# Kernel optimization log

Measured on AMD Instinct MI355X. Metric: run time of the kernel, lower is better.

The kernel has to match this reference:

```python
import jax, jax.numpy as jnp
import numpy as np

B, S, HID = 2, 1024, 2048
H, KV, D = 32, 8, 64          # heads, kv heads, head_dim
G = H // KV                    # GQA groups
THETA = 10000.0


def _rope_cos_sin(seq_len):
    # (S, D/2) cos/sin tables, interleaved-pair RoPE
    freqs = 1.0 / THETA ** (jnp.arange(0, D, 2, dtype=jnp.float32) / D)
    t = jnp.arange(seq_len, dtype=jnp.float32)
    f = jnp.outer(t, freqs)
    return jnp.cos(f), jnp.sin(f)


def _apply_rope(x, cos, sin):
    # x: (B, S, h, D); cos/sin: (S, D/2) -> broadcast (1, S, 1, D/2)
    c = cos[None, :, None, :]
    s = sin[None, :, None, :]
    xe, xo = x[..., ::2], x[..., 1::2]
    oe = xe * c - xo * s
    oo = xo * c + xe * s
    # re-interleave even/odd
    return jnp.stack([oe, oo], axis=-1).reshape(x.shape)


def setup_inputs() -> dict:
    key = jax.random.key(0)
    ks = jax.random.split(key, 5)
    return {
        "hidden_states": jax.random.normal(ks[0], (B, S, HID), jnp.float32),
        "Wq": jax.random.normal(ks[1], (HID, H * D), jnp.float32) * 0.02,
        "Wk": jax.random.normal(ks[2], (HID, KV * D), jnp.float32) * 0.02,
        "Wv": jax.random.normal(ks[3], (HID, KV * D), jnp.float32) * 0.02,
        "Wo": jax.random.normal(ks[4], (H * D, HID), jnp.float32) * 0.02,
    }


def reference(hidden_states, Wq, Wk, Wv, Wo):
    b, s, _ = hidden_states.shape
    q = (hidden_states @ Wq).reshape(b, s, H, D)
    k = (hidden_states @ Wk).reshape(b, s, KV, D)
    v = (hidden_states @ Wv).reshape(b, s, KV, D)

    cos, sin = _rope_cos_sin(s)
    q = _apply_rope(q, cos, sin)
    k = _apply_rope(k, cos, sin)

    # GQA: repeat kv heads to match query heads
    k = jnp.repeat(k, G, axis=2)  # (b, s, H, D)
    v = jnp.repeat(v, G, axis=2)

    scale = jnp.sqrt(jnp.float32(D))
    scores = jnp.einsum("bqhd,bkhd->bhqk", q, k) / scale  # (b, H, s, s)
    causal = jnp.tril(jnp.ones((s, s), jnp.float32))[None, None]
    scores = jnp.where(causal < 0.5, jnp.float32(-1e10), scores)
    weights = jax.nn.softmax(scores, axis=-1)
    ctx = jnp.einsum("bhqk,bkhd->bqhd", weights, v).reshape(b, s, H * D)
    return ctx @ Wo
```

## Files before the change

kernel.cpp:

```cpp
#include <hip/hip_runtime.h>
#include <hip/hip_bf16.h>

typedef __attribute__((ext_vector_type(8))) __bf16 bf16x8;
typedef __attribute__((ext_vector_type(4))) float f32x4;

#define MFMA16(a,b,c) __builtin_amdgcn_mfma_f32_16x16x32_bf16(a,b,c,0,0,0)

__device__ __forceinline__ unsigned short f2b(float x){
  __hip_bfloat16 h = __float2bfloat16(x);
  return __builtin_bit_cast(unsigned short, h);
}

__device__ __forceinline__ void gload16(const unsigned short* g, unsigned short* l){
  __builtin_amdgcn_global_load_lds(
      (const __attribute__((address_space(1))) unsigned int*)g,
      (__attribute__((address_space(3))) unsigned int*)l, 16, 0, 0);
}

__global__ void k_rope_table(float* __restrict__ ct, float* __restrict__ st){
  int i = blockIdx.x*256 + threadIdx.x;
  int t = i >> 5, f = i & 31;
  float freq = powf(10000.0f, -(float)f/32.0f);
  float a = (float)t * freq;
  ct[i] = cosf(a);
  st[i] = sinf(a);
}

__global__ void k_cvt(const float* __restrict__ src, unsigned short* __restrict__ dst, int n4){
  int i = blockIdx.x*256 + threadIdx.x;
  int stride = gridDim.x*256;
  for (; i < n4; i += stride){
    float4 v = ((const float4*)src)[i];
    ushort4 o; o.x=f2b(v.x); o.y=f2b(v.y); o.z=f2b(v.z); o.w=f2b(v.w);
    ((ushort4*)dst)[i] = o;
  }
}

__global__ __launch_bounds__(256) void k_prep_wt(
    const float* __restrict__ Wq, const float* __restrict__ Wk,
    const float* __restrict__ Wv, unsigned short* __restrict__ Wt){
  __shared__ float t[32][33];
  int n0 = blockIdx.x*32, k0 = blockIdx.y*32;
  const float* src; int N, nl;
  if (n0 < 2048)      { src=Wq; N=2048; nl=n0; }
  else if (n0 < 2560) { src=Wk; N=512;  nl=n0-2048; }
  else                { src=Wv; N=512;  nl=n0-2560; }
  int r = threadIdx.x>>5, c = threadIdx.x&31;
  #pragma unroll
  for (int it=0; it<4; ++it)
    t[r+8*it][c] = src[(size_t)(k0+r+8*it)*N + nl + c];
  __syncthreads();
  #pragma unroll
  for (int it=0; it<4; ++it)
    Wt[(size_t)(n0+r+8*it)*2048 + k0 + c] = f2b(t[c][r+8*it]);
}

__global__ __launch_bounds__(256) void k_prep_wo(
    const float* __restrict__ Wo, unsigned short* __restrict__ Wot){
  __shared__ float t[32][33];
  int n0 = blockIdx.x*32, k0 = blockIdx.y*32;
  int r = threadIdx.x>>5, c = threadIdx.x&31;
  #pragma unroll
  for (int it=0; it<4; ++it)
    t[r+8*it][c] = Wo[(size_t)(k0+r+8*it)*2048 + n0 + c];
  __syncthreads();
  #pragma unroll
  for (int it=0; it<4; ++it)
    Wot[(size_t)(n0+r+8*it)*2048 + k0 + c] = f2b(t[c][r+8*it]);
}

__global__ __launch_bounds__(256) void k_qkv(
    const unsigned short* __restrict__ A, const unsigned short* __restrict__ Bt,
    const float* __restrict__ ct, const float* __restrict__ st,
    unsigned short* __restrict__ qb, unsigned short* __restrict__ kb,
    unsigned short* __restrict__ vt)
{
  __shared__ unsigned short As[3][128*32];
  __shared__ unsigned short Bs[3][64*32];
  const int mt = blockIdx.x & 15;
  const int nt = blockIdx.x >> 4;
  const int bm = mt*128, bn_g = nt*64;
  const int tid=threadIdx.x, wave=tid>>6, lane=tid&63;
  const int lrow=lane&15, kgrp=lane>>4;
  const int wm=(wave>>1)*64, wn=(wave&1)*32;
  const int arow = tid>>2;
  const int acs  = (((tid&3) ^ ((tid>>3)&3)))*8;
  const int ksw  = (kgrp ^ ((lrow>>1)&3))*8;
  f32x4 acc[4][2] = {};

  #define STAGE_Q(buf, k0) do {                                                               \
    gload16(&A [(size_t)(bm + arow     )*2048 + (k0) + acs], &As[buf][(wave*64)*8]);          \
    gload16(&A [(size_t)(bm + 64 + arow)*2048 + (k0) + acs], &As[buf][(256 + wave*64)*8]);    \
    gload16(&Bt[(size_t)(bn_g + arow   )*2048 + (k0) + acs], &Bs[buf][(wave*64)*8]);          \
  } while(0)

  #define COMPUTE_Q(buf) do {                                          \
    bf16x8 a0,a1,a2,a3,b0,b1;                                          \
    a0 = *(const bf16x8*)&As[buf][(wm+ 0+lrow)*32 + ksw];              \
    a1 = *(const bf16x8*)&As[buf][(wm+16+lrow)*32 + ksw];              \
    a2 = *(const bf16x8*)&As[buf][(wm+32+lrow)*32 + ksw];              \
    a3 = *(const bf16x8*)&As[buf][(wm+48+lrow)*32 + ksw];              \
    b0 = *(const bf16x8*)&Bs[buf][(wn+ 0+lrow)*32 + ksw];              \
    b1 = *(const bf16x8*)&Bs[buf][(wn+16+lrow)*32 + ksw];              \
    acc[0][0]=MFMA16(a0,b0,acc[0][0]); acc[0][1]=MFMA16(a0,b1,acc[0][1]); \
    acc[1][0]=MFMA16(a1,b0,acc[1][0]); acc[1][1]=MFMA16(a1,b1,acc[1][1]); \
    acc[2][0]=MFMA16(a2,b0,acc[2][0]); acc[2][1]=MFMA16(a2,b1,acc[2][1]); \
    acc[3][0]=MFMA16(a3,b0,acc[3][0]); acc[3][1]=MFMA16(a3,b1,acc[3][1]); \
  } while(0)

  STAGE_Q(0, 0);
  STAGE_Q(1, 32);
  int cur = 0;
  #pragma unroll 1
  for (int t=0; t<64; ++t){
    asm volatile("s_waitcnt vmcnt(3)" ::: "memory");
    __builtin_amdgcn_s_barrier();
    int kn = t+2; if (kn > 63) kn = 63;
    int nb = cur+2; if (nb > 2) nb -= 3;
    STAGE_Q(nb, kn*32);
    COMPUTE_Q(cur);
    cur = (cur==2) ? 0 : cur+1;
  }

  const int wtype = (bn_g < 2048) ? 0 : (bn_g < 2560 ? 1 : 2);
  #pragma unroll
  for (int mi=0;mi<4;mi++){
    #pragma unroll
    for (int ni=0;ni<2;ni++){
      int gr0 = bm + wm + mi*16 + kgrp*4;
      int gc  = bn_g + wn + ni*16 + lrow;
      if (wtype==2){
        int c = gc - 2560;
        int bq = gr0 >> 10, s0 = gr0 & 1023;
        ushort4 o;
        o.x=f2b(acc[mi][ni][0]); o.y=f2b(acc[mi][ni][1]);
        o.z=f2b(acc[mi][ni][2]); o.w=f2b(acc[mi][ni][3]);
        *(ushort4*)&vt[((size_t)(bq*512 + c))*1024 + s0] = o;
      } else {
        int d = gc & 63, fi = d >> 1, odd = d & 1;
        #pragma unroll
        for (int r=0;r<4;r++){
          float x = acc[mi][ni][r];
          float p = __shfl_xor(x, 1, 64);
          int srow = (gr0 + r) & 1023;
          float c = ct[srow*32 + fi], sn = st[srow*32 + fi];
          float o = odd ? (x*c + p*sn) : (x*c - p*sn);
          if (wtype==0) qb[(size_t)(gr0+r)*2048 + gc] = f2b(o*0.125f);
          else          kb[(size_t)(gr0+r)*512 + (gc-2048)] = f2b(o);
        }
      }
    }
  }
  #undef STAGE_Q
  #undef COMPUTE_Q
}

#define LDP 72
__global__ __launch_bounds__(256) void k_attn(
    const unsigned short* __restrict__ qb, const unsigned short* __restrict__ kb,
    const unsigned short* __restrict__ vt, unsigned short* __restrict__ ctxb)
{
  __shared__ unsigned short Ks[3][64*LDP];
  __shared__ unsigned short Vs[3][64*LDP];
  __shared__ unsigned short QP[64*LDP];

  const int p  = blockIdx.x >> 6;
  const int bh = blockIdx.x & 63;
  const int h  = bh & 31;
  const int b  = bh >> 5;
  const int kvh = h >> 2;

  const int tid=threadIdx.x, wave=tid>>6, lane=tid&63;
  const int lrow=lane&15, kgrp=lane>>4;
  const int wq = wave*16;
  const int sr = tid>>2, seg = (tid&3)*16;

  const unsigned short* kbase = kb + (size_t)(b*1024)*512 + kvh*64 + seg;
  const unsigned short* vbase = vt + ((size_t)(b*512 + kvh*64 + sr))*1024 + seg;

  #pragma unroll
  for (int phase=0; phase<2; ++phase){
    const int qt = phase==0 ? 15-p : p;
    const int q0 = qt*64;

    __syncthreads();
    {
      const unsigned short* src = qb + (size_t)(b*1024 + q0 + sr)*2048 + h*64 + seg;
      *(uint4*)&QP[sr*LDP + seg]     = *(const uint4*)&src[0];
      *(uint4*)&QP[sr*LDP + seg + 8] = *(const uint4*)&src[8];
      const unsigned short* ksrc = kbase + (size_t)sr*512;
      *(uint4*)&Ks[0][sr*LDP + seg]     = *(const uint4*)&ksrc[0];
      *(uint4*)&Ks[0][sr*LDP + seg + 8] = *(const uint4*)&ksrc[8];
      *(uint4*)&Vs[0][sr*LDP + seg]     = *(const uint4*)&vbase[0];
      *(uint4*)&Vs[0][sr*LDP + seg + 8] = *(const uint4*)&vbase[8];
    }
    __syncthreads();

    bf16x8 qa[2];
    #pragma unroll
    for (int ks=0;ks<2;ks++)
      qa[ks] = *(const bf16x8*)&QP[(wq+lrow)*LDP + ks*32 + kgrp*8];

    float m_run = -1e30f, l_run = 0.f;
    f32x4 out[4] = {};

    for (int j=0;j<=qt;j++){
      const int cb = j%3;
      uint4 kra, krb, vra, vrb;
      if (j < qt){
        const unsigned short* ksrc = kbase + (size_t)((j+1)*64 + sr)*512;
        kra = *(const uint4*)&ksrc[0]; krb = *(const uint4*)&ksrc[8];
        const unsigned short* vsrc = vbase + (j+1)*64;
        vra = *(const uint4*)&vsrc[0]; vrb = *(const uint4*)&vsrc[8];
      }

      f32x4 sc[4] = {};
      #pragma unroll
      for (int ks=0;ks<2;ks++){
        #pragma unroll
        for (int ni=0;ni<4;ni++){
          bf16x8 kf = *(const bf16x8*)&Ks[cb][(ni*16+lrow)*LDP + ks*32 + kgrp*8];
          sc[ni] = MFMA16(kf, qa[ks], sc[ni]);
        }
      }

      if (j == qt){
        #pragma unroll
        for (int ni=0;ni<4;ni++)
          #pragma unroll
          for (int r=0;r<4;r++)
            if (ni*16 + kgrp*4 + r > wq + lrow) sc[ni][r] = -1e30f;
      }

      float mx = sc[0][0];
      #pragma unroll
      for (int ni=0;ni<4;ni++)
        #pragma unroll
        for (int r=0;r<4;r++) mx = fmaxf(mx, sc[ni][r]);
      mx = fmaxf(mx, __shfl_xor(mx, 16, 64));
      mx = fmaxf(mx, __shfl_xor(mx, 32, 64));
      float mnew = fmaxf(m_run, mx);
      float corr = __expf(m_run - mnew);
      m_run = mnew;
      float rsum = 0.f;
      #pragma unroll
      for (int ni=0;ni<4;ni++)
        #pragma unroll
        for (int r=0;r<4;r++){
          float pv = __expf(sc[ni][r] - mnew);
          sc[ni][r] = pv;
          rsum += pv;
        }
      rsum += __shfl_xor(rsum, 16, 64);
      rsum += __shfl_xor(rsum, 32, 64);
      l_run = l_run*corr + rsum;
      #pragma unroll
      for (int di=0;di<4;di++)
        #pragma unroll
        for (int r=0;r<4;r++) out[di][r] *= corr;

      #pragma unroll
      for (int ni=0;ni<4;ni++){
        ushort4 o;
        o.x=f2b(sc[ni][0]); o.y=f2b(sc[ni][1]);
        o.z=f2b(sc[ni][2]); o.w=f2b(sc[ni][3]);
        *(ushort4*)&QP[(wq+lrow)*LDP + ni*16 + kgrp*4] = o;
      }

      #pragma unroll
      for (int ks2=0;ks2<2;ks2++){
        bf16x8 pb = *(const bf16x8*)&QP[(wq+lrow)*LDP + ks2*32 + kgrp*8];
        #pragma unroll
        for (int di=0;di<4;di++){
          bf16x8 vf = *(const bf16x8*)&Vs[cb][(di*16+lrow)*LDP + ks2*32 + kgrp*8];
          out[di] = MFMA16(vf, pb, out[di]);
        }
      }

      if (j < qt){
        const int nb = (j+1)%3;
        *(uint4*)&Ks[nb][sr*LDP + seg]     = kra;
        *(uint4*)&Ks[nb][sr*LDP + seg + 8] = krb;
        *(uint4*)&Vs[nb][sr*LDP + seg]     = vra;
        *(uint4*)&Vs[nb][sr*LDP + seg + 8] = vrb;
      }
      __syncthreads();
    }

    float rl = 1.0f / l_run;
    #pragma unroll
    for (int di=0;di<4;di++){
      ushort4 o;
      o.x=f2b(out[di][0]*rl); o.y=f2b(out[di][1]*rl);
      o.z=f2b(out[di][2]*rl); o.w=f2b(out[di][3]*rl);
      *(ushort4*)&ctxb[(size_t)(b*1024 + q0 + wq + lrow)*2048
                       + h*64 + di*16 + kgrp*4] = o;
    }
  }
}

__global__ __launch_bounds__(256) void k_oproj(
    const unsigned short* __restrict__ A, const unsigned short* __restrict__ Bt,
    float* __restrict__ out)
{
  __shared__ unsigned short As[3][128*32];
  __shared__ unsigned short Bs[3][64*32];
  const int mt = blockIdx.x & 15;
  const int nt = blockIdx.x >> 4;
  const int bm = mt*128, bn = nt*64;
  const int tid=threadIdx.x, wave=tid>>6, lane=tid&63;
  const int lrow=lane&15, kgrp=lane>>4;
  const int wm=(wave>>1)*64, wn=(wave&1)*32;
  const int arow = tid>>2;
  const int acs  = (((tid&3) ^ ((tid>>3)&3)))*8;
  const int ksw  = (kgrp ^ ((lrow>>1)&3))*8;
  f32x4 acc[4][2] = {};

  #define STAGE_O(buf, k0) do {                                                               \
    gload16(&A [(size_t)(bm + arow     )*2048 + (k0) + acs], &As[buf][(wave*64)*8]);          \
    gload16(&A [(size_t)(bm + 64 + arow)*2048 + (k0) + acs], &As[buf][(256 + wave*64)*8]);    \
    gload16(&Bt[(size_t)(bn + arow     )*2048 + (k0) + acs], &Bs[buf][(wave*64)*8]);          \
  } while(0)

  #define COMPUTE_O(buf) do {                                          \
    bf16x8 a0,a1,a2,a3,b0,b1;                                          \
    a0 = *(const bf16x8*)&As[buf][(wm+ 0+lrow)*32 + ksw];              \
    a1 = *(const bf16x8*)&As[buf][(wm+16+lrow)*32 + ksw];              \
    a2 = *(const bf16x8*)&As[buf][(wm+32+lrow)*32 + ksw];              \
    a3 = *(const bf16x8*)&As[buf][(wm+48+lrow)*32 + ksw];              \
    b0 = *(const bf16x8*)&Bs[buf][(wn+ 0+lrow)*32 + ksw];              \
    b1 = *(const bf16x8*)&Bs[buf][(wn+16+lrow)*32 + ksw];              \
    acc[0][0]=MFMA16(a0,b0,acc[0][0]); acc[0][1]=MFMA16(a0,b1,acc[0][1]); \
    acc[1][0]=MFMA16(a1,b0,acc[1][0]); acc[1][1]=MFMA16(a1,b1,acc[1][1]); \
    acc[2][0]=MFMA16(a2,b0,acc[2][0]); acc[2][1]=MFMA16(a2,b1,acc[2][1]); \
    acc[3][0]=MFMA16(a3,b0,acc[3][0]); acc[3][1]=MFMA16(a3,b1,acc[3][1]); \
  } while(0)

  STAGE_O(0, 0);
  STAGE_O(1, 32);
  int cur = 0;
  #pragma unroll 1
  for (int t=0; t<64; ++t){
    asm volatile("s_waitcnt vmcnt(3)" ::: "memory");
    __builtin_amdgcn_s_barrier();
    int kn = t+2; if (kn > 63) kn = 63;
    int nb = cur+2; if (nb > 2) nb -= 3;
    STAGE_O(nb, kn*32);
    COMPUTE_O(cur);
    cur = (cur==2) ? 0 : cur+1;
  }

  #pragma unroll
  for (int mi=0;mi<4;mi++)
    #pragma unroll
    for (int ni=0;ni<2;ni++){
      int gr0 = bm + wm + mi*16 + kgrp*4;
      int gc  = bn + wn + ni*16 + lrow;
      #pragma unroll
      for (int r=0;r<4;r++)
        out[(size_t)(gr0+r)*2048 + gc] = acc[mi][ni][r];
    }
  #undef STAGE_O
  #undef COMPUTE_O
}

extern "C" void kernel_launch(void* const* d_in, const int* in_sizes, int n_in,
                              void* d_out, int out_size, void* d_ws, size_t ws_size,
                              hipStream_t stream)
{
  const float* X  = (const float*)d_in[0];
  const float* Wq = (const float*)d_in[1];
  const float* Wk = (const float*)d_in[2];
  const float* Wv = (const float*)d_in[3];
  const float* Wo = (const float*)d_in[4];
  float* out = (float*)d_out;
  char* ws = (char*)d_ws;

  const size_t MB = 1048576;
  float* ct = (float*)ws;
  float* st = (float*)(ws + 128*1024);
  unsigned short* Xb   = (unsigned short*)(ws + 256*1024);
  unsigned short* Wt   = (unsigned short*)(ws + 256*1024 + 8*MB);
  unsigned short* Wot  = (unsigned short*)(ws + 256*1024 + 20*MB);
  unsigned short* qb   = (unsigned short*)(ws + 256*1024 + 28*MB);
  unsigned short* kb   = (unsigned short*)(ws + 256*1024 + 36*MB);
  unsigned short* vt   = (unsigned short*)(ws + 256*1024 + 38*MB);
  unsigned short* ctxb = (unsigned short*)(ws + 256*1024 + 40*MB);

  hipLaunchKernelGGL(k_rope_table, dim3(128), dim3(256), 0, stream, ct, st);
  hipLaunchKernelGGL(k_cvt, dim3(2048), dim3(256), 0, stream, X, Xb, 2048*2048/4);
  hipLaunchKernelGGL(k_prep_wt, dim3(96,64), dim3(256), 0, stream, Wq, Wk, Wv, Wt);
  hipLaunchKernelGGL(k_prep_wo, dim3(64,64), dim3(256), 0, stream, Wo, Wot);
  hipLaunchKernelGGL(k_qkv, dim3(768), dim3(256), 0, stream,
                     Xb, Wt, ct, st, qb, kb, vt);
  hipLaunchKernelGGL(k_attn, dim3(512), dim3(256), 0, stream, qb, kb, vt, ctxb);
  hipLaunchKernelGGL(k_oproj, dim3(512), dim3(256), 0, stream, ctxb, Wot, out);
}
```

Baseline: 142.1 us.

## Deepen GEMM pipelines, remap blocks per XCD, and lazily rescale softmax in exp2

The QKV and output-projection GEMMs move from three LDS stages to four, with three loads in flight, and remap block indices so that blocks sharing N tiles land on the same XCD for better L2 reuse. The attention kernel folds log2(e) into the Q scale so it can use exp2f, and skips the online-softmax rescale unless the max grows by more than a threshold. It also groups the query heads of one KV head onto the same XCD, cuts K/V buffering to two stages, and raises wave priority around the MFMA blocks. These changes target memory latency, cache locality and softmax ALU cost, at the price of more LDS in the GEMMs and relying on a bounded-growth threshold for numerical safety.

```diff
diff --git a/kernel.cpp b/kernel.cpp
--- a/kernel.cpp
+++ b/kernel.cpp
@@ -75,10 +75,11 @@
     unsigned short* __restrict__ qb, unsigned short* __restrict__ kb,
     unsigned short* __restrict__ vt)
 {
-  __shared__ unsigned short As[3][128*32];
-  __shared__ unsigned short Bs[3][64*32];
-  const int mt = blockIdx.x & 15;
-  const int nt = blockIdx.x >> 4;
+  __shared__ unsigned short As[4][128*32];
+  __shared__ unsigned short Bs[4][64*32];
+  const int xcd = blockIdx.x & 7, idx = blockIdx.x >> 3;
+  const int mt = idx & 15;
+  const int nt = xcd*6 + (idx >> 4);
   const int bm = mt*128, bn_g = nt*64;
   const int tid=threadIdx.x, wave=tid>>6, lane=tid&63;
   const int lrow=lane&15, kgrp=lane>>4;
@@ -110,19 +111,18 @@
 
   STAGE_Q(0, 0);
   STAGE_Q(1, 32);
-  int cur = 0;
+  STAGE_Q(2, 64);
   #pragma unroll 1
   for (int t=0; t<64; ++t){
-    asm volatile("s_waitcnt vmcnt(3)" ::: "memory");
+    asm volatile("s_waitcnt vmcnt(6)" ::: "memory");
     __builtin_amdgcn_s_barrier();
-    int kn = t+2; if (kn > 63) kn = 63;
-    int nb = cur+2; if (nb > 2) nb -= 3;
-    STAGE_Q(nb, kn*32);
-    COMPUTE_Q(cur);
-    cur = (cur==2) ? 0 : cur+1;
+    int kn = t+3; if (kn > 63) kn = 63;
+    STAGE_Q((t+3)&3, kn*32);
+    COMPUTE_Q(t&3);
   }
 
   const int wtype = (bn_g < 2048) ? 0 : (bn_g < 2560 ? 1 : 2);
+  const float qscale = 0.125f * 1.44269504f;
   #pragma unroll
   for (int mi=0;mi<4;mi++){
     #pragma unroll
@@ -145,7 +145,7 @@
           int srow = (gr0 + r) & 1023;
           float c = ct[srow*32 + fi], sn = st[srow*32 + fi];
           float o = odd ? (x*c + p*sn) : (x*c - p*sn);
-          if (wtype==0) qb[(size_t)(gr0+r)*2048 + gc] = f2b(o*0.125f);
+          if (wtype==0) qb[(size_t)(gr0+r)*2048 + gc] = f2b(o*qscale);
           else          kb[(size_t)(gr0+r)*512 + (gc-2048)] = f2b(o);
         }
       }
@@ -160,15 +160,16 @@
     const unsigned short* __restrict__ qb, const unsigned short* __restrict__ kb,
     const unsigned short* __restrict__ vt, unsigned short* __restrict__ ctxb)
 {
-  __shared__ unsigned short Ks[3][64*LDP];
-  __shared__ unsigned short Vs[3][64*LDP];
+  __shared__ unsigned short Ks[2][64*LDP];
+  __shared__ unsigned short Vs[2][64*LDP];
   __shared__ unsigned short QP[64*LDP];
 
-  const int p  = blockIdx.x >> 6;
-  const int bh = blockIdx.x & 63;
-  const int h  = bh & 31;
-  const int b  = bh >> 5;
-  const int kvh = h >> 2;
+  const int kvh = blockIdx.x & 7;
+  const int s   = blockIdx.x >> 3;
+  const int b   = s >> 5;
+  const int hh  = (s >> 3) & 3;
+  const int p   = s & 7;
+  const int h   = kvh*4 + hh;
 
   const int tid=threadIdx.x, wave=tid>>6, lane=tid&63;
   const int lrow=lane&15, kgrp=lane>>4;
@@ -205,7 +206,7 @@
     f32x4 out[4] = {};
 
     for (int j=0;j<=qt;j++){
-      const int cb = j%3;
+      const int cb = j&1;
       uint4 kra, krb, vra, vrb;
       if (j < qt){
         const unsigned short* ksrc = kbase + (size_t)((j+1)*64 + sr)*512;
@@ -215,6 +216,7 @@
       }
 
       f32x4 sc[4] = {};
+      __builtin_amdgcn_s_setprio(1);
       #pragma unroll
       for (int ks=0;ks<2;ks++){
         #pragma unroll
@@ -223,6 +225,7 @@
           sc[ni] = MFMA16(kf, qa[ks], sc[ni]);
         }
       }
+      __builtin_amdgcn_s_setprio(0);
 
       if (j == qt){
         #pragma unroll
@@ -239,25 +242,28 @@
         for (int r=0;r<4;r++) mx = fmaxf(mx, sc[ni][r]);
       mx = fmaxf(mx, __shfl_xor(mx, 16, 64));
       mx = fmaxf(mx, __shfl_xor(mx, 32, 64));
-      float mnew = fmaxf(m_run, mx);
-      float corr = __expf(m_run - mnew);
-      m_run = mnew;
+      if (__any(mx > m_run + 12.0f)){
+        float mnew = fmaxf(m_run, mx);
+        float corr = exp2f(m_run - mnew);
+        m_run = mnew;
+        l_run *= corr;
+        #pragma unroll
+        for (int di=0;di<4;di++)
+          #pragma unroll
+          for (int r=0;r<4;r++) out[di][r] *= corr;
+      }
       float rsum = 0.f;
       #pragma unroll
       for (int ni=0;ni<4;ni++)
         #pragma unroll
         for (int r=0;r<4;r++){
-          float pv = __expf(sc[ni][r] - mnew);
+          float pv = exp2f(sc[ni][r] - m_run);
           sc[ni][r] = pv;
           rsum += pv;
         }
       rsum += __shfl_xor(rsum, 16, 64);
       rsum += __shfl_xor(rsum, 32, 64);
-      l_run = l_run*corr + rsum;
-      #pragma unroll
-      for (int di=0;di<4;di++)
-        #pragma unroll
-        for (int r=0;r<4;r++) out[di][r] *= corr;
+      l_run += rsum;
 
       #pragma unroll
       for (int ni=0;ni<4;ni++){
@@ -267,6 +273,7 @@
         *(ushort4*)&QP[(wq+lrow)*LDP + ni*16 + kgrp*4] = o;
       }
 
+      __builtin_amdgcn_s_setprio(1);
       #pragma unroll
       for (int ks2=0;ks2<2;ks2++){
         bf16x8 pb = *(const bf16x8*)&QP[(wq+lrow)*LDP + ks2*32 + kgrp*8];
@@ -276,9 +283,10 @@
           out[di] = MFMA16(vf, pb, out[di]);
         }
       }
+      __builtin_amdgcn_s_setprio(0);
 
       if (j < qt){
-        const int nb = (j+1)%3;
+        const int nb = (j+1)&1;
         *(uint4*)&Ks[nb][sr*LDP + seg]     = kra;
         *(uint4*)&Ks[nb][sr*LDP + seg + 8] = krb;
         *(uint4*)&Vs[nb][sr*LDP + seg]     = vra;
@@ -303,10 +311,11 @@
     const unsigned short* __restrict__ A, const unsigned short* __restrict__ Bt,
     float* __restrict__ out)
 {
-  __shared__ unsigned short As[3][128*32];
-  __shared__ unsigned short Bs[3][64*32];
-  const int mt = blockIdx.x & 15;
-  const int nt = blockIdx.x >> 4;
+  __shared__ unsigned short As[4][128*32];
+  __shared__ unsigned short Bs[4][64*32];
+  const int xcd = blockIdx.x & 7, idx = blockIdx.x >> 3;
+  const int mt = idx & 15;
+  const int nt = xcd*4 + (idx >> 4);
   const int bm = mt*128, bn = nt*64;
   const int tid=threadIdx.x, wave=tid>>6, lane=tid&63;
   const int lrow=lane&15, kgrp=lane>>4;
@@ -338,16 +347,14 @@
 
   STAGE_O(0, 0);
   STAGE_O(1, 32);
-  int cur = 0;
+  STAGE_O(2, 64);
   #pragma unroll 1
   for (int t=0; t<64; ++t){
-    asm volatile("s_waitcnt vmcnt(3)" ::: "memory");
+    asm volatile("s_waitcnt vmcnt(6)" ::: "memory");
     __builtin_amdgcn_s_barrier();
-    int kn = t+2; if (kn > 63) kn = 63;
-    int nb = cur+2; if (nb > 2) nb -= 3;
-    STAGE_O(nb, kn*32);
-    COMPUTE_O(cur);
-    cur = (cur==2) ? 0 : cur+1;
+    int kn = t+3; if (kn > 63) kn = 63;
+    STAGE_O((t+3)&3, kn*32);
+    COMPUTE_O(t&3);
   }
 
   #pragma unroll
```

Measured after the change: 145.4 us. 1.02x slower.
